# Optimization experiments

Hardware: AMD Instinct MI355X
Metric: run time of the kernel (lower is better)

The kernel has to match this reference:

```python
import jax, jax.numpy as jnp
import numpy as np

B, T, V, E, H, L = 128, 128, 5000, 256, 512, 128
PAD_IDX = 0


def setup_inputs() -> dict:
    key = jax.random.key(0)
    ks = jax.random.split(key, 12)
    s = 0.02  # init scale
    noise = jax.random.normal(ks[0], (B, L), dtype=jnp.float32)
    # Precomputed gumbel noise, one draw per (step, batch, vocab)
    u = jax.random.uniform(ks[1], (T, B, V), dtype=jnp.float32, minval=1e-9, maxval=1.0)
    gumbel = -jnp.log(-jnp.log(u))
    emb = (jax.random.normal(ks[2], (V, E), dtype=jnp.float32) * s).at[PAD_IDX].set(0.0)
    return {
        "noise": noise,
        "gumbel": gumbel,
        "temperature": jnp.float32(1.0),
        "W_init": jax.random.normal(ks[3], (H, L), dtype=jnp.float32) * s,
        "b_init": jnp.zeros((H,), dtype=jnp.float32),
        "emb": emb,
        "W_ih": jax.random.normal(ks[4], (3 * H, E), dtype=jnp.float32) * s,
        "W_hh": jax.random.normal(ks[5], (3 * H, H), dtype=jnp.float32) * s,
        "b_ih": jax.random.normal(ks[6], (3 * H,), dtype=jnp.float32) * s,
        "b_hh": jax.random.normal(ks[7], (3 * H,), dtype=jnp.float32) * s,
        "W_out": jax.random.normal(ks[8], (V, H), dtype=jnp.float32) * s,
        "b_out": jnp.zeros((V,), dtype=jnp.float32),
    }


def reference(noise, gumbel, temperature, W_init, b_init, emb, W_ih, W_hh, b_ih, b_hh, W_out, b_out):
    # h_0 = fc_initial_state(noise)  -> [B, H]
    h0 = noise @ W_init.T + b_init
    # first-step input: one-hot at pad_idx (embedding row PAD_IDX, which is zero)
    onehot0 = jnp.zeros((B, V), dtype=noise.dtype).at[:, PAD_IDX].set(1.0)
    tau = jnp.reshape(temperature, ())

    def step(carry, g):
        h, prev_onehot = carry
        x = prev_onehot @ emb                      # [B, E] soft-embedding feedback
        gi = x @ W_ih.T + b_ih                     # [B, 3H]
        gh = h @ W_hh.T + b_hh                     # [B, 3H]
        i_r, i_z, i_n = jnp.split(gi, 3, axis=-1)
        h_r, h_z, h_n = jnp.split(gh, 3, axis=-1)
        r = jax.nn.sigmoid(i_r + h_r)
        z = jax.nn.sigmoid(i_z + h_z)
        n = jnp.tanh(i_n + r * h_n)
        h_new = (1.0 - z) * n + z * h              # GRU cell (torch convention)
        # dropout is identity in eval mode
        logits = h_new @ W_out.T + b_out           # [B, V]
        y = jax.nn.softmax((logits + g) / tau, axis=-1)  # soft gumbel-softmax
        return (h_new, y), y

    _, ys = jax.lax.scan(step, (h0, onehot0), gumbel)  # ys: [T, B, V]
    return jnp.transpose(ys, (1, 0, 2))                # [B, T, V]
```

## Files before the change

kernel.cpp:

```cpp
#include <hip/hip_runtime.h>
#include <math.h>

#define Bq 128
#define Tq 128
#define Vq 5000
#define VP 5120
#define Eq 256
#define Hq 512
#define Lq 128
#define G3H 1536
#define KT 128
#define LROW 136

typedef __attribute__((ext_vector_type(8))) short bf16x8;
typedef __attribute__((ext_vector_type(4))) float f32x4;

__device__ __forceinline__ ushort f2bf(float f) {
    union { float f; unsigned u; } v; v.f = f;
    unsigned r = (v.u + 0x7FFFu + ((v.u >> 16) & 1u)) >> 16;
    return (ushort)r;
}
__device__ __forceinline__ float bf2f(ushort s) {
    union { unsigned u; float f; } v; v.u = ((unsigned)s) << 16;
    return v.f;
}

template<int MI>
__device__ __forceinline__ void macT(
    f32x4 (&acc)[MI][4],
    const ushort* __restrict__ A, int lda,
    const ushort* __restrict__ Bm, int ldb,
    int n0, int kbase, int Klen,
    ushort* As, ushort* Bs)
{
    const int NA = 2 * MI;
    const int tid = threadIdx.x;
    const int lane = tid & 63;
    const int w = tid >> 6;
    const int wm = (w >> 1) * (MI * 16);
    const int wn = (w & 1) * 64;
    const int fr = lane & 15;
    const int fk = (lane >> 4) * 8;

    int arow[NA], akc[NA];
    #pragma unroll
    for (int i = 0; i < NA; ++i) {
        int c = tid + i * 256;
        arow[i] = c >> 4; akc[i] = (c & 15) * 8;
    }
    int brow[8], bkc[8];
    #pragma unroll
    for (int i = 0; i < 8; ++i) {
        int c = tid + i * 256;
        brow[i] = c >> 4; bkc[i] = (c & 15) * 8;
    }

    const int nk = Klen / KT;
    bf16x8 ra[NA], rb[8];
    #pragma unroll
    for (int i = 0; i < NA; ++i)
        ra[i] = *(const bf16x8*)(A + (size_t)arow[i] * lda + kbase + akc[i]);
    #pragma unroll
    for (int i = 0; i < 8; ++i)
        rb[i] = *(const bf16x8*)(Bm + (size_t)(n0 + brow[i]) * ldb + kbase + bkc[i]);
    #pragma unroll
    for (int i = 0; i < NA; ++i)
        *(bf16x8*)(As + arow[i] * LROW + akc[i]) = ra[i];
    #pragma unroll
    for (int i = 0; i < 8; ++i)
        *(bf16x8*)(Bs + brow[i] * LROW + bkc[i]) = rb[i];
    __syncthreads();

    for (int kt = 0; kt < nk; ++kt) {
        if (kt + 1 < nk) {
            int kb = kbase + (kt + 1) * KT;
            #pragma unroll
            for (int i = 0; i < NA; ++i)
                ra[i] = *(const bf16x8*)(A + (size_t)arow[i] * lda + kb + akc[i]);
            #pragma unroll
            for (int i = 0; i < 8; ++i)
                rb[i] = *(const bf16x8*)(Bm + (size_t)(n0 + brow[i]) * ldb + kb + bkc[i]);
        }
        #pragma unroll
        for (int ks = 0; ks < 4; ++ks) {
            bf16x8 af[MI], bfv[4];
            const int ko = ks * 32 + fk;
            #pragma unroll
            for (int mi = 0; mi < MI; ++mi)
                af[mi] = *(const bf16x8*)(As + (wm + mi * 16 + fr) * LROW + ko);
            #pragma unroll
            for (int ni = 0; ni < 4; ++ni)
                bfv[ni] = *(const bf16x8*)(Bs + (wn + ni * 16 + fr) * LROW + ko);
            #pragma unroll
            for (int mi = 0; mi < MI; ++mi)
                #pragma unroll
                for (int ni = 0; ni < 4; ++ni)
                    acc[mi][ni] = __builtin_amdgcn_mfma_f32_16x16x32_bf16(
                        af[mi], bfv[ni], acc[mi][ni], 0, 0, 0);
        }
        __syncthreads();
        if (kt + 1 < nk) {
            #pragma unroll
            for (int i = 0; i < NA; ++i)
                *(bf16x8*)(As + arow[i] * LROW + akc[i]) = ra[i];
            #pragma unroll
            for (int i = 0; i < 8; ++i)
                *(bf16x8*)(Bs + brow[i] * LROW + bkc[i]) = rb[i];
            __syncthreads();
        }
    }
}

__global__ __launch_bounds__(256) void k_prep(
    const float* __restrict__ W_ih, const float* __restrict__ W_hh,
    const float* __restrict__ W_out, const float* __restrict__ noise,
    const float* __restrict__ W_init, const float* __restrict__ emb,
    ushort* __restrict__ WihB, ushort* __restrict__ WhhB, ushort* __restrict__ WoutB,
    ushort* __restrict__ noiseB, ushort* __restrict__ WinitB,
    ushort* __restrict__ embB, ushort* __restrict__ yE)
{
    const int tg = blockIdx.x * 256 + threadIdx.x;
    const int NTH = gridDim.x * 256;
    for (int i = tg; i < G3H * Eq / 4; i += NTH) {
        float4 f = *(const float4*)(W_ih + (size_t)i * 4);
        *(ushort4*)(WihB + (size_t)i * 4) =
            make_ushort4(f2bf(f.x), f2bf(f.y), f2bf(f.z), f2bf(f.w));
    }
    for (int i = tg; i < G3H * Hq / 4; i += NTH) {
        float4 f = *(const float4*)(W_hh + (size_t)i * 4);
        *(ushort4*)(WhhB + (size_t)i * 4) =
            make_ushort4(f2bf(f.x), f2bf(f.y), f2bf(f.z), f2bf(f.w));
    }
    for (int i = tg; i < VP * (Hq / 4); i += NTH) {
        int v = i >> 7, h4 = (i & 127) << 2;
        ushort4 o = make_ushort4(0, 0, 0, 0);
        if (v < Vq) {
            float4 f = *(const float4*)(W_out + (size_t)v * Hq + h4);
            o = make_ushort4(f2bf(f.x), f2bf(f.y), f2bf(f.z), f2bf(f.w));
        }
        *(ushort4*)(WoutB + (size_t)v * Hq + h4) = o;
    }
    for (int i = tg; i < VP * (Eq / 4); i += NTH) {
        int v = i >> 6, e4 = (i & 63) << 2;
        ushort4 o = make_ushort4(0, 0, 0, 0);
        if (v < Vq) {
            float4 f = *(const float4*)(emb + (size_t)v * Eq + e4);
            o = make_ushort4(f2bf(f.x), f2bf(f.y), f2bf(f.z), f2bf(f.w));
        }
        *(ushort4*)(embB + (size_t)v * Eq + e4) = o;
    }
    for (int i = tg; i < Bq * Lq / 4; i += NTH) {
        float4 f = *(const float4*)(noise + (size_t)i * 4);
        *(ushort4*)(noiseB + (size_t)i * 4) =
            make_ushort4(f2bf(f.x), f2bf(f.y), f2bf(f.z), f2bf(f.w));
    }
    for (int i = tg; i < Hq * Lq / 4; i += NTH) {
        float4 f = *(const float4*)(W_init + (size_t)i * 4);
        *(ushort4*)(WinitB + (size_t)i * 4) =
            make_ushort4(f2bf(f.x), f2bf(f.y), f2bf(f.z), f2bf(f.w));
    }
    for (int i = tg; i < Bq * (VP / 4); i += NTH) {
        int v4 = i % (VP / 4);
        ushort4 o = (v4 == 0) ? make_ushort4(0x3F80, 0, 0, 0)
                              : make_ushort4(0, 0, 0, 0);
        *(ushort4*)(yE + (size_t)i * 4) = o;
    }
}

__global__ __launch_bounds__(256) void k_wh0(
    const ushort* __restrict__ WihB, const ushort* __restrict__ embB,
    const ushort* __restrict__ noiseB, const ushort* __restrict__ WinitB,
    const float* __restrict__ b_init,
    ushort* __restrict__ WcombT, float* __restrict__ h0, ushort* __restrict__ hB0)
{
    __shared__ __align__(16) ushort As[128 * LROW];
    __shared__ __align__(16) ushort Bs[128 * LROW];
    const int bid = blockIdx.x;
    const int lane = threadIdx.x & 63;
    const int w = threadIdx.x >> 6;
    const int wm = (w >> 1) * 64, wn = (w & 1) * 64;
    const int fr = lane & 15, hi = lane >> 4;
    f32x4 acc[4][4];
    #pragma unroll
    for (int mi = 0; mi < 4; ++mi)
        #pragma unroll
        for (int ni = 0; ni < 4; ++ni) acc[mi][ni] = (f32x4){0.f,0.f,0.f,0.f};
    if (bid < 480) {
        int mt = bid / 40, nt = bid % 40;
        macT<4>(acc, WihB + (size_t)mt * 128 * Eq, Eq, embB, Eq,
                nt * 128, 0, Eq, As, Bs);
        #pragma unroll
        for (int mi = 0; mi < 4; ++mi)
            #pragma unroll
            for (int ni = 0; ni < 4; ++ni) {
                int n = nt * 128 + wn + ni * 16 + fr;
                #pragma unroll
                for (int r = 0; r < 4; ++r) {
                    int m = mt * 128 + wm + mi * 16 + hi * 4 + r;
                    WcombT[(size_t)m * VP + n] = f2bf(acc[mi][ni][r]);
                }
            }
    } else {
        int n0 = (bid - 480) * 128;
        macT<4>(acc, noiseB, Lq, WinitB, Lq, n0, 0, Lq, As, Bs);
        #pragma unroll
        for (int mi = 0; mi < 4; ++mi)
            #pragma unroll
            for (int ni = 0; ni < 4; ++ni) {
                int n = n0 + wn + ni * 16 + fr;
                float bv = b_init[n];
                #pragma unroll
                for (int r = 0; r < 4; ++r) {
                    int m = wm + mi * 16 + hi * 4 + r;
                    float v = acc[mi][ni][r] + bv;
                    h0[(size_t)m * Hq + n] = v;
                    hB0[(size_t)m * Hq + n] = f2bf(v);
                }
            }
    }
}

__global__ __launch_bounds__(256) void k_gi(
    const ushort* __restrict__ yE, const ushort* __restrict__ WcombT,
    const ushort* __restrict__ hB_old, const ushort* __restrict__ WhhB,
    ushort* __restrict__ gip, ushort* __restrict__ ghp,
    float* __restrict__ out, const float* __restrict__ esumAll, int t)
{
    __shared__ __align__(16) ushort As[128 * LROW];
    __shared__ __align__(16) ushort Bs[128 * LROW];
    const int bid = blockIdx.x;
    const int lane = threadIdx.x & 63, w = threadIdx.x >> 6;
    const int fr = lane & 15, hi = lane >> 4;
    if (bid < 384) {
        const int nt = bid >> 5;
        const int r5 = bid & 31;
        const int mq = r5 >> 3;
        const int z = r5 & 7;
        const int wm = (w >> 1) * 16, wn = (w & 1) * 64;
        const int n0 = nt * 128;
        f32x4 acc[1][4];
        #pragma unroll
        for (int ni = 0; ni < 4; ++ni) acc[0][ni] = (f32x4){0.f,0.f,0.f,0.f};
        macT<1>(acc, yE + (size_t)mq * 32 * VP, VP, WcombT, VP,
                n0, z * 640, 640, As, Bs);
        ushort* C = gip + (size_t)z * (Bq * G3H) + (size_t)mq * 32 * G3H;
        #pragma unroll
        for (int ni = 0; ni < 4; ++ni) {
            int n = n0 + wn + ni * 16 + fr;
            #pragma unroll
            for (int r = 0; r < 4; ++r) {
                int m = wm + hi * 4 + r;
                C[(size_t)m * G3H + n] = f2bf(acc[0][ni][r]);
            }
        }
    } else if (bid < 408) {
        const int j = bid - 384, nt = j >> 1, kc = j & 1;
        const int wm = (w >> 1) * 64, wn = (w & 1) * 64;
        const int n0 = nt * 128;
        f32x4 acc[4][4];
        #pragma unroll
        for (int mi = 0; mi < 4; ++mi)
            #pragma unroll
            for (int ni = 0; ni < 4; ++ni) acc[mi][ni] = (f32x4){0.f,0.f,0.f,0.f};
        macT<4>(acc, hB_old, Hq, WhhB, Hq, n0, kc * 256, 256, As, Bs);
        ushort* C = ghp + (size_t)kc * (Bq * G3H);
        #pragma unroll
        for (int mi = 0; mi < 4; ++mi)
            #pragma unroll
            for (int ni = 0; ni < 4; ++ni) {
                int n = n0 + wn + ni * 16 + fr;
                #pragma unroll
                for (int r = 0; r < 4; ++r) {
                    int m = wm + mi * 16 + hi * 4 + r;
                    C[(size_t)m * G3H + n] = f2bf(acc[mi][ni][r]);
                }
            }
    } else if (t > 0) {
        const int tid = threadIdx.x;
        #pragma unroll
        for (int j = 0; j < 2; ++j) {
            int b = (bid - 408) * 2 + j;
            float S = 0.f;
            #pragma unroll 8
            for (int nt = 0; nt < 40; ++nt)
                S += esumAll[(size_t)(t - 1) * 5120 + nt * 128 + b];
            float inv = 1.0f / S;
            float* orow = out + ((size_t)b * Tq + (t - 1)) * Vq;
            #pragma unroll
            for (int i = 0; i < 20; ++i) {
                int v = tid + i * 256;
                if (v < Vq) orow[v] *= inv;
            }
        }
    }
}

__global__ __launch_bounds__(256) void k_gates(
    const ushort* __restrict__ gip, const ushort* __restrict__ ghp,
    const float* __restrict__ b_ih, const float* __restrict__ b_hh,
    const float* __restrict__ h_old, const float* __restrict__ esumAll,
    float* __restrict__ h_new, ushort* __restrict__ hB_new, int t)
{
    __shared__ float sred[64];
    const int tid = threadIdx.x;
    const int e = blockIdx.x * 256 + tid;
    const int b = e >> 9, i = e & 511;
    if (t > 0) {
        if (tid < 40) sred[tid] = esumAll[(size_t)(t - 1) * 5120 + tid * 128 + b];
        __syncthreads();
        if (tid == 0) {
            float S = 0.f;
            #pragma unroll
            for (int nt = 0; nt < 40; ++nt) S += sred[nt];
            sred[63] = 1.0f / S;
        }
        __syncthreads();
    } else {
        if (tid == 0) sred[63] = 1.0f;
        __syncthreads();
    }
    const float invS = sred[63];

    const size_t o = (size_t)b * G3H + i;
    float xr = 0.f, xz = 0.f, xn = 0.f;
    #pragma unroll
    for (int z = 0; z < 8; ++z) {
        const ushort* gp = gip + (size_t)z * (Bq * G3H) + o;
        xr += bf2f(gp[0]); xz += bf2f(gp[Hq]); xn += bf2f(gp[2 * Hq]);
    }
    xr = xr * invS + b_ih[i];
    xz = xz * invS + b_ih[Hq + i];
    xn = xn * invS + b_ih[2 * Hq + i];
    const ushort* h0p = ghp + o;
    const ushort* h1p = ghp + (size_t)(Bq * G3H) + o;
    float hr = b_hh[i] + bf2f(h0p[0]) + bf2f(h1p[0]);
    float hz = b_hh[Hq + i] + bf2f(h0p[Hq]) + bf2f(h1p[Hq]);
    float hn = b_hh[2 * Hq + i] + bf2f(h0p[2 * Hq]) + bf2f(h1p[2 * Hq]);
    float r = 1.f / (1.f + expf(-(xr + hr)));
    float zz = 1.f / (1.f + expf(-(xz + hz)));
    float nn = tanhf(xn + r * hn);
    float hv = (1.f - zz) * nn + zz * h_old[e];
    h_new[e] = hv;
    hB_new[e] = f2bf(hv);
}

__global__ __launch_bounds__(256) void k_logits(
    const ushort* __restrict__ hB, const ushort* __restrict__ WoutB,
    const float* __restrict__ b_out, const float* __restrict__ gum,
    const float* __restrict__ temp,
    float* __restrict__ out, ushort* __restrict__ yE,
    float* __restrict__ esumAll, int t)
{
    __shared__ __align__(16) ushort As[32 * LROW];
    __shared__ __align__(16) ushort Bs[128 * LROW];
    const int tid = threadIdx.x;
    const int nt = blockIdx.x >> 2;
    const int mbase = (blockIdx.x & 3) * 32;
    const int n0 = nt * 128;
    const int lane = tid & 63, w = tid >> 6;
    const int wm = (w >> 1) * 16, wn = (w & 1) * 64;
    const int fr = lane & 15, hi = lane >> 4;
    const float inv_tau = 1.0f / temp[0];
    f32x4 acc[1][4];
    #pragma unroll
    for (int ni = 0; ni < 4; ++ni) acc[0][ni] = (f32x4){0.f,0.f,0.f,0.f};
    macT<1>(acc, hB + (size_t)mbase * Hq, Hq, WoutB, Hq, n0, 0, Hq, As, Bs);

    float psum[4] = {0.f, 0.f, 0.f, 0.f};
    #pragma unroll
    for (int ni = 0; ni < 4; ++ni) {
        int v = n0 + wn + ni * 16 + fr;
        bool valid = v < Vq;
        float bo = valid ? b_out[v] : 0.f;
        #pragma unroll
        for (int r = 0; r < 4; ++r) {
            int m = mbase + wm + hi * 4 + r;
            float ev = 0.f;
            if (valid) {
                float g = gum[(size_t)m * Vq + v];
                ev = expf((acc[0][ni][r] + bo + g) * inv_tau);
                out[(size_t)m * Tq * Vq + (size_t)t * Vq + v] = ev;
            }
            yE[(size_t)m * VP + v] = f2bf(ev);
            psum[r] += ev;
        }
    }
    float* redbuf = (float*)As;
    #pragma unroll
    for (int r = 0; r < 4; ++r) {
        float s = psum[r];
        s += __shfl_xor(s, 1); s += __shfl_xor(s, 2);
        s += __shfl_xor(s, 4); s += __shfl_xor(s, 8);
        if (fr == 0)
            redbuf[((wm + hi * 4 + r) << 1) | (wn >> 6)] = s;
    }
    __syncthreads();
    if (tid < 32)
        esumAll[(size_t)t * 5120 + n0 + mbase + tid]
            = redbuf[tid * 2] + redbuf[tid * 2 + 1];
}

__global__ __launch_bounds__(256) void k_tail(
    float* __restrict__ out, const float* __restrict__ esumAll)
{
    const int tid = threadIdx.x;
    #pragma unroll
    for (int j = 0; j < 4; ++j) {
        int b = blockIdx.x * 4 + j;
        float S = 0.f;
        #pragma unroll 8
        for (int nt = 0; nt < 40; ++nt)
            S += esumAll[(size_t)(Tq - 1) * 5120 + nt * 128 + b];
        float inv = 1.0f / S;
        float* orow = out + ((size_t)b * Tq + (Tq - 1)) * Vq;
        #pragma unroll
        for (int i = 0; i < 20; ++i) {
            int v = tid + i * 256;
            if (v < Vq) orow[v] *= inv;
        }
    }
}

extern "C" void kernel_launch(void* const* d_in, const int* in_sizes, int n_in,
                              void* d_out, int out_size, void* d_ws, size_t ws_size,
                              hipStream_t stream)
{
    const float* noise   = (const float*)d_in[0];
    const float* gumbel  = (const float*)d_in[1];
    const float* temp    = (const float*)d_in[2];
    const float* W_init  = (const float*)d_in[3];
    const float* b_init  = (const float*)d_in[4];
    const float* emb     = (const float*)d_in[5];
    const float* W_ih    = (const float*)d_in[6];
    const float* W_hh    = (const float*)d_in[7];
    const float* b_ih    = (const float*)d_in[8];
    const float* b_hh    = (const float*)d_in[9];
    const float* W_out   = (const float*)d_in[10];
    const float* b_out   = (const float*)d_in[11];
    float* out = (float*)d_out;

    float* fbase   = (float*)d_ws;
    float* h       = fbase;
    float* esumAll = h + 2 * 65536;
    ushort* ub     = (ushort*)(esumAll + 655360);
    ushort* gip    = ub;
    ushort* ghp    = gip + 1572864;
    ushort* embB   = ghp + 393216;
    ushort* WihB   = embB + 1310720;
    ushort* WhhB   = WihB + 393216;
    ushort* WoutB  = WhhB + 786432;
    ushort* WcombT = WoutB + 2621440;
    ushort* noiseB = WcombT + 7864320;
    ushort* WinitB = noiseB + 16384;
    ushort* hB     = WinitB + 65536;
    ushort* yE     = hB + 2 * 65536;

    k_prep<<<dim3(512), dim3(256), 0, stream>>>(
        W_ih, W_hh, W_out, noise, W_init, emb,
        WihB, WhhB, WoutB, noiseB, WinitB, embB, yE);
    k_wh0<<<dim3(484), dim3(256), 0, stream>>>(
        WihB, embB, noiseB, WinitB, b_init, WcombT, h, hB);

    for (int t = 0; t < Tq; ++t) {
        float* h_old = h + (size_t)(t & 1) * 65536;
        float* h_new = h + (size_t)((t + 1) & 1) * 65536;
        ushort* hB_old = hB + (size_t)(t & 1) * 65536;
        ushort* hB_new = hB + (size_t)((t + 1) & 1) * 65536;

        k_gi<<<dim3(472), dim3(256), 0, stream>>>(
            yE, WcombT, hB_old, WhhB, gip, ghp, out, esumAll, t);
        k_gates<<<dim3(256), dim3(256), 0, stream>>>(
            gip, ghp, b_ih, b_hh, h_old, esumAll, h_new, hB_new, t);
        k_logits<<<dim3(160), dim3(256), 0, stream>>>(
            hB_new, WoutB, b_out, gumbel + (size_t)t * Bq * Vq, temp,
            out, yE, esumAll, t);
    }
    k_tail<<<dim3(32), dim3(256), 0, stream>>>(out, esumAll);
}
```

Measured before the change: 3.513 ms.

## Move next-step hidden GEMM and prior-step normalization into logits kernel

The h@W_hh GEMM for the next step is now computed inside k_logits from the freshly produced hidden state, running alongside the output projection blocks. The deferred softmax normalization of the previous step also moves there, leaving k_gi with only the soft-embedding GEMM. Both GEMMs now use 64-row tiles instead of 32 or 128, which changes the block counts. This shortens the critical path of k_gi and fills idle CUs during k_logits, at the cost of a larger, more heterogeneous logits launch. The k_gi path for the hidden GEMM only runs at t==0.

```diff
diff --git a/kernel.cpp b/kernel.cpp
--- a/kernel.cpp
+++ b/kernel.cpp
@@ -223,75 +223,56 @@
 __global__ __launch_bounds__(256) void k_gi(
     const ushort* __restrict__ yE, const ushort* __restrict__ WcombT,
     const ushort* __restrict__ hB_old, const ushort* __restrict__ WhhB,
-    ushort* __restrict__ gip, ushort* __restrict__ ghp,
-    float* __restrict__ out, const float* __restrict__ esumAll, int t)
-{
-    __shared__ __align__(16) ushort As[128 * LROW];
+    ushort* __restrict__ gip, ushort* __restrict__ ghp, int t)
+{
+    __shared__ __align__(16) ushort As[64 * LROW];
     __shared__ __align__(16) ushort Bs[128 * LROW];
     const int bid = blockIdx.x;
     const int lane = threadIdx.x & 63, w = threadIdx.x >> 6;
     const int fr = lane & 15, hi = lane >> 4;
-    if (bid < 384) {
-        const int nt = bid >> 5;
-        const int r5 = bid & 31;
-        const int mq = r5 >> 3;
-        const int z = r5 & 7;
-        const int wm = (w >> 1) * 16, wn = (w & 1) * 64;
+    const int wm = (w >> 1) * 32, wn = (w & 1) * 64;
+    f32x4 acc[2][4];
+    #pragma unroll
+    for (int mi = 0; mi < 2; ++mi)
+        #pragma unroll
+        for (int ni = 0; ni < 4; ++ni) acc[mi][ni] = (f32x4){0.f,0.f,0.f,0.f};
+    if (bid < 192) {
+        const int nt = bid >> 4, rem = bid & 15;
+        const int mh = rem >> 3, z = rem & 7;
         const int n0 = nt * 128;
-        f32x4 acc[1][4];
-        #pragma unroll
-        for (int ni = 0; ni < 4; ++ni) acc[0][ni] = (f32x4){0.f,0.f,0.f,0.f};
-        macT<1>(acc, yE + (size_t)mq * 32 * VP, VP, WcombT, VP,
+        macT<2>(acc, yE + (size_t)mh * 64 * VP, VP, WcombT, VP,
                 n0, z * 640, 640, As, Bs);
-        ushort* C = gip + (size_t)z * (Bq * G3H) + (size_t)mq * 32 * G3H;
-        #pragma unroll
-        for (int ni = 0; ni < 4; ++ni) {
-            int n = n0 + wn + ni * 16 + fr;
-            #pragma unroll
-            for (int r = 0; r < 4; ++r) {
-                int m = wm + hi * 4 + r;
-                C[(size_t)m * G3H + n] = f2bf(acc[0][ni][r]);
-            }
-        }
-    } else if (bid < 408) {
-        const int j = bid - 384, nt = j >> 1, kc = j & 1;
-        const int wm = (w >> 1) * 64, wn = (w & 1) * 64;
-        const int n0 = nt * 128;
-        f32x4 acc[4][4];
-        #pragma unroll
-        for (int mi = 0; mi < 4; ++mi)
-            #pragma unroll
-            for (int ni = 0; ni < 4; ++ni) acc[mi][ni] = (f32x4){0.f,0.f,0.f,0.f};
-        macT<4>(acc, hB_old, Hq, WhhB, Hq, n0, kc * 256, 256, As, Bs);
-        ushort* C = ghp + (size_t)kc * (Bq * G3H);
-        #pragma unroll
-        for (int mi = 0; mi < 4; ++mi)
+        ushort* C = gip + (size_t)z * (Bq * G3H);
+        #pragma unroll
+        for (int mi = 0; mi < 2; ++mi)
             #pragma unroll
             for (int ni = 0; ni < 4; ++ni) {
                 int n = n0 + wn + ni * 16 + fr;
                 #pragma unroll
                 for (int r = 0; r < 4; ++r) {
-                    int m = wm + mi * 16 + hi * 4 + r;
+                    int m = mh * 64 + wm + mi * 16 + hi * 4 + r;
                     C[(size_t)m * G3H + n] = f2bf(acc[mi][ni][r]);
                 }
             }
-    } else if (t > 0) {
-        const int tid = threadIdx.x;
-        #pragma unroll
-        for (int j = 0; j < 2; ++j) {
-            int b = (bid - 408) * 2 + j;
-            float S = 0.f;
-            #pragma unroll 8
-            for (int nt = 0; nt < 40; ++nt)
-                S += esumAll[(size_t)(t - 1) * 5120 + nt * 128 + b];
-            float inv = 1.0f / S;
-            float* orow = out + ((size_t)b * Tq + (t - 1)) * Vq;
-            #pragma unroll
-            for (int i = 0; i < 20; ++i) {
-                int v = tid + i * 256;
-                if (v < Vq) orow[v] *= inv;
-            }
-        }
+    } else if (t == 0) {
+        const int j = bid - 192;
+        const int nt = j >> 2, rem = j & 3;
+        const int mh = rem >> 1, kc = rem & 1;
+        const int n0 = nt * 128;
+        macT<2>(acc, hB_old + (size_t)mh * 64 * Hq, Hq, WhhB, Hq,
+                n0, kc * 256, 256, As, Bs);
+        ushort* C = ghp + (size_t)kc * (Bq * G3H);
+        #pragma unroll
+        for (int mi = 0; mi < 2; ++mi)
+            #pragma unroll
+            for (int ni = 0; ni < 4; ++ni) {
+                int n = n0 + wn + ni * 16 + fr;
+                #pragma unroll
+                for (int r = 0; r < 4; ++r) {
+                    int m = mh * 64 + wm + mi * 16 + hi * 4 + r;
+                    C[(size_t)m * G3H + n] = f2bf(acc[mi][ni][r]);
+                }
+            }
     }
 }
 
@@ -346,58 +327,103 @@
 
 __global__ __launch_bounds__(256) void k_logits(
     const ushort* __restrict__ hB, const ushort* __restrict__ WoutB,
+    const ushort* __restrict__ WhhB,
     const float* __restrict__ b_out, const float* __restrict__ gum,
     const float* __restrict__ temp,
     float* __restrict__ out, ushort* __restrict__ yE,
-    float* __restrict__ esumAll, int t)
-{
-    __shared__ __align__(16) ushort As[32 * LROW];
+    float* __restrict__ esumAll, ushort* __restrict__ ghp, int t)
+{
+    __shared__ __align__(16) ushort As[64 * LROW];
     __shared__ __align__(16) ushort Bs[128 * LROW];
+    const int bid = blockIdx.x;
     const int tid = threadIdx.x;
-    const int nt = blockIdx.x >> 2;
-    const int mbase = (blockIdx.x & 3) * 32;
-    const int n0 = nt * 128;
     const int lane = tid & 63, w = tid >> 6;
-    const int wm = (w >> 1) * 16, wn = (w & 1) * 64;
     const int fr = lane & 15, hi = lane >> 4;
-    const float inv_tau = 1.0f / temp[0];
-    f32x4 acc[1][4];
-    #pragma unroll
-    for (int ni = 0; ni < 4; ++ni) acc[0][ni] = (f32x4){0.f,0.f,0.f,0.f};
-    macT<1>(acc, hB + (size_t)mbase * Hq, Hq, WoutB, Hq, n0, 0, Hq, As, Bs);
-
-    float psum[4] = {0.f, 0.f, 0.f, 0.f};
-    #pragma unroll
-    for (int ni = 0; ni < 4; ++ni) {
-        int v = n0 + wn + ni * 16 + fr;
-        bool valid = v < Vq;
-        float bo = valid ? b_out[v] : 0.f;
+    if (bid < 160) {
+        const int nt = bid >> 2;
+        const int mbase = (bid & 3) * 32;
+        const int n0 = nt * 128;
+        const int wm = (w >> 1) * 16, wn = (w & 1) * 64;
+        const float inv_tau = 1.0f / temp[0];
+        f32x4 acc[1][4];
+        #pragma unroll
+        for (int ni = 0; ni < 4; ++ni) acc[0][ni] = (f32x4){0.f,0.f,0.f,0.f};
+        macT<1>(acc, hB + (size_t)mbase * Hq, Hq, WoutB, Hq, n0, 0, Hq, As, Bs);
+
+        float psum[4] = {0.f, 0.f, 0.f, 0.f};
+        #pragma unroll
+        for (int ni = 0; ni < 4; ++ni) {
+            int v = n0 + wn + ni * 16 + fr;
+            bool valid = v < Vq;
+            float bo = valid ? b_out[v] : 0.f;
+            #pragma unroll
+            for (int r = 0; r < 4; ++r) {
+                int m = mbase + wm + hi * 4 + r;
+                float ev = 0.f;
+                if (valid) {
+                    float g = gum[(size_t)m * Vq + v];
+                    ev = expf((acc[0][ni][r] + bo + g) * inv_tau);
+                    out[(size_t)m * Tq * Vq + (size_t)t * Vq + v] = ev;
+                }
+                yE[(size_t)m * VP + v] = f2bf(ev);
+                psum[r] += ev;
+            }
+        }
+        float* redbuf = (float*)As;
         #pragma unroll
         for (int r = 0; r < 4; ++r) {
-            int m = mbase + wm + hi * 4 + r;
-            float ev = 0.f;
-            if (valid) {
-                float g = gum[(size_t)m * Vq + v];
-                ev = expf((acc[0][ni][r] + bo + g) * inv_tau);
-                out[(size_t)m * Tq * Vq + (size_t)t * Vq + v] = ev;
-            }
-            yE[(size_t)m * VP + v] = f2bf(ev);
-            psum[r] += ev;
-        }
-    }
-    float* redbuf = (float*)As;
-    #pragma unroll
-    for (int r = 0; r < 4; ++r) {
-        float s = psum[r];
-        s += __shfl_xor(s, 1); s += __shfl_xor(s, 2);
-        s += __shfl_xor(s, 4); s += __shfl_xor(s, 8);
-        if (fr == 0)
-            redbuf[((wm + hi * 4 + r) << 1) | (wn >> 6)] = s;
-    }
-    __syncthreads();
-    if (tid < 32)
-        esumAll[(size_t)t * 5120 + n0 + mbase + tid]
-            = redbuf[tid * 2] + redbuf[tid * 2 + 1];
+            float s = psum[r];
+            s += __shfl_xor(s, 1); s += __shfl_xor(s, 2);
+            s += __shfl_xor(s, 4); s += __shfl_xor(s, 8);
+            if (fr == 0)
+                redbuf[((wm + hi * 4 + r) << 1) | (wn >> 6)] = s;
+        }
+        __syncthreads();
+        if (tid < 32)
+            esumAll[(size_t)t * 5120 + n0 + mbase + tid]
+                = redbuf[tid * 2] + redbuf[tid * 2 + 1];
+    } else if (bid < 208) {
+        const int j = bid - 160;
+        const int nt = j >> 2, rem = j & 3;
+        const int mh = rem >> 1, kc = rem & 1;
+        const int n0 = nt * 128;
+        const int wm = (w >> 1) * 32, wn = (w & 1) * 64;
+        f32x4 acc[2][4];
+        #pragma unroll
+        for (int mi = 0; mi < 2; ++mi)
+            #pragma unroll
+            for (int ni = 0; ni < 4; ++ni) acc[mi][ni] = (f32x4){0.f,0.f,0.f,0.f};
+        macT<2>(acc, hB + (size_t)mh * 64 * Hq, Hq, WhhB, Hq,
+                n0, kc * 256, 256, As, Bs);
+        ushort* C = ghp + (size_t)kc * (Bq * G3H);
+        #pragma unroll
+        for (int mi = 0; mi < 2; ++mi)
+            #pragma unroll
+            for (int ni = 0; ni < 4; ++ni) {
+                int n = n0 + wn + ni * 16 + fr;
+                #pragma unroll
+                for (int r = 0; r < 4; ++r) {
+                    int m = mh * 64 + wm + mi * 16 + hi * 4 + r;
+                    C[(size_t)m * G3H + n] = f2bf(acc[mi][ni][r]);
+                }
+            }
+    } else if (t > 0) {
+        #pragma unroll
+        for (int j = 0; j < 2; ++j) {
+            int b = (bid - 208) * 2 + j;
+            float S = 0.f;
+            #pragma unroll 8
+            for (int nt2 = 0; nt2 < 40; ++nt2)
+                S += esumAll[(size_t)(t - 1) * 5120 + nt2 * 128 + b];
+            float inv = 1.0f / S;
+            float* orow = out + ((size_t)b * Tq + (t - 1)) * Vq;
+            #pragma unroll
+            for (int i = 0; i < 20; ++i) {
+                int v = tid + i * 256;
+                if (v < Vq) orow[v] *= inv;
+            }
+        }
+    }
 }
 
 __global__ __launch_bounds__(256) void k_tail(
@@ -467,13 +493,13 @@
         ushort* hB_old = hB + (size_t)(t & 1) * 65536;
         ushort* hB_new = hB + (size_t)((t + 1) & 1) * 65536;
 
-        k_gi<<<dim3(472), dim3(256), 0, stream>>>(
-            yE, WcombT, hB_old, WhhB, gip, ghp, out, esumAll, t);
+        k_gi<<<dim3(t == 0 ? 240 : 192), dim3(256), 0, stream>>>(
+            yE, WcombT, hB_old, WhhB, gip, ghp, t);
         k_gates<<<dim3(256), dim3(256), 0, stream>>>(
             gip, ghp, b_ih, b_hh, h_old, esumAll, h_new, hB_new, t);
-        k_logits<<<dim3(160), dim3(256), 0, stream>>>(
-            hB_new, WoutB, b_out, gumbel + (size_t)t * Bq * Vq, temp,
-            out, yE, esumAll, t);
+        k_logits<<<dim3(272), dim3(256), 0, stream>>>(
+            hB_new, WoutB, WhhB, b_out, gumbel + (size_t)t * Bq * Vq, temp,
+            out, yE, esumAll, ghp, t);
     }
     k_tail<<<dim3(32), dim3(256), 0, stream>>>(out, esumAll);
 }
```

Result: no change. 3.583 ms (+2.0%).

## Fuse GRU gates into logits kernel via in-kernel atomic barrier

Applied to the files above, without the earlier changes.

Merges the gate-update kernel into the logits kernel: 8 blocks compute the GRU state and signal through an atomic counter, while the 160 logits blocks spin-wait on per-group flags before running their GEMM. This removes one kernel launch per timestep (128 in total). The W_hh GEMM is also split across more, smaller blocks (48 instead of 24), with a smaller shared-memory A tile. The risk is that the spin-wait deadlocks or stalls if the producer blocks are not co-resident. The gate work is also concentrated in only 8 blocks, so that phase gets less parallelism.

```diff
diff --git a/kernel.cpp b/kernel.cpp
--- a/kernel.cpp
+++ b/kernel.cpp
@@ -111,6 +111,234 @@
     }
 }
 
+
+__device__ __forceinline__ void gi_block(
+    int bid, const ushort* __restrict__ yE, const ushort* __restrict__ WcombT,
+    ushort* __restrict__ gip, ushort* As, ushort* Bs)
+{
+    const int tid = threadIdx.x;
+    const int lane = tid & 63, w = tid >> 6;
+    const int fr = lane & 15, hi = lane >> 4;
+    const int nt = bid >> 5, rem = bid & 31;
+    const int mq = rem >> 3, z = rem & 7;
+    const int wm = (w >> 1) * 16, wn = (w & 1) * 64;
+    const int n0 = nt * 128;
+    f32x4 acc[1][4];
+    #pragma unroll
+    for (int ni = 0; ni < 4; ++ni) acc[0][ni] = (f32x4){0.f,0.f,0.f,0.f};
+    macT<1>(acc, yE + (size_t)mq * 32 * VP, VP, WcombT, VP,
+            n0, z * 640, 640, As, Bs);
+    ushort* C = gip + (size_t)z * (Bq * G3H) + (size_t)mq * 32 * G3H;
+    #pragma unroll
+    for (int ni = 0; ni < 4; ++ni) {
+        int n = n0 + wn + ni * 16 + fr;
+        #pragma unroll
+        for (int r = 0; r < 4; ++r) {
+            int m = wm + hi * 4 + r;
+            C[(size_t)m * G3H + n] = f2bf(acc[0][ni][r]);
+        }
+    }
+}
+
+__device__ __forceinline__ void gh_block(
+    int j, const ushort* __restrict__ hBsrc, const ushort* __restrict__ WhhB,
+    ushort* __restrict__ ghp, ushort* As, ushort* Bs)
+{
+    const int tid = threadIdx.x;
+    const int lane = tid & 63, w = tid >> 6;
+    const int fr = lane & 15, hi = lane >> 4;
+    const int nt = j >> 2, rem = j & 3;
+    const int mh = rem >> 1, kc = rem & 1;
+    const int n0 = nt * 128;
+    const int wm = (w >> 1) * 32, wn = (w & 1) * 64;
+    f32x4 acc[2][4];
+    #pragma unroll
+    for (int mi = 0; mi < 2; ++mi)
+        #pragma unroll
+        for (int ni = 0; ni < 4; ++ni) acc[mi][ni] = (f32x4){0.f,0.f,0.f,0.f};
+    macT<2>(acc, hBsrc + (size_t)mh * 64 * Hq, Hq, WhhB, Hq,
+            n0, kc * 256, 256, As, Bs);
+    ushort* C = ghp + (size_t)kc * (Bq * G3H);
+    #pragma unroll
+    for (int mi = 0; mi < 2; ++mi)
+        #pragma unroll
+        for (int ni = 0; ni < 4; ++ni) {
+            int n = n0 + wn + ni * 16 + fr;
+            #pragma unroll
+            for (int r = 0; r < 4; ++r) {
+                int m = mh * 64 + wm + mi * 16 + hi * 4 + r;
+                C[(size_t)m * G3H + n] = f2bf(acc[mi][ni][r]);
+            }
+        }
+}
+
+__device__ __forceinline__ void norm2(
+    int bpair, int tprev, float* __restrict__ out,
+    const float* __restrict__ esumAll)
+{
+    const int tid = threadIdx.x;
+    #pragma unroll
+    for (int j = 0; j < 2; ++j) {
+        int b = bpair * 2 + j;
+        float S = 0.f;
+        #pragma unroll 8
+        for (int nt = 0; nt < 40; ++nt)
+            S += esumAll[(size_t)tprev * 5120 + nt * 128 + b];
+        float inv = 1.0f / S;
+        float* orow = out + ((size_t)b * Tq + tprev) * Vq;
+        #pragma unroll
+        for (int i = 0; i < 20; ++i) {
+            int v = tid + i * 256;
+            if (v < Vq) orow[v] *= inv;
+        }
+    }
+}
+
+__global__ __launch_bounds__(256) void k_s1(
+    const ushort* __restrict__ yE, const ushort* __restrict__ WcombT,
+    const ushort* __restrict__ hB_old, const ushort* __restrict__ WhhB,
+    ushort* __restrict__ gip, ushort* __restrict__ ghp,
+    float* __restrict__ out, const float* __restrict__ esumAll, int t)
+{
+    __shared__ __align__(16) ushort As[64 * LROW];
+    __shared__ __align__(16) ushort Bs[128 * LROW];
+    const int bid = blockIdx.x;
+    if (bid < 384)
+        gi_block(bid, yE, WcombT, gip, As, Bs);
+    else if (bid < 432)
+        gh_block(bid - 384, hB_old, WhhB, ghp, As, Bs);
+    else if (t > 0)
+        norm2(bid - 432, t - 1, out, esumAll);
+}
+
+__global__ __launch_bounds__(256) void k_gl(
+    const ushort* __restrict__ gip, const ushort* __restrict__ ghp,
+    const float* __restrict__ b_ih, const float* __restrict__ b_hh,
+    const float* __restrict__ h_old, float* __restrict__ h_new,
+    ushort* __restrict__ hB_new,
+    const ushort* __restrict__ WoutB, const float* __restrict__ b_out,
+    const float* __restrict__ gum, const float* __restrict__ temp,
+    float* __restrict__ out, ushort* __restrict__ yE,
+    float* __restrict__ esumAll, unsigned* __restrict__ bar, int t)
+{
+    __shared__ __align__(16) ushort As[32 * LROW];
+    __shared__ __align__(16) ushort Bs[128 * LROW];
+    __shared__ float invS_sh[16];
+    const int tid = threadIdx.x;
+    const int bid = blockIdx.x;
+
+    if (bid < 8) {
+        const int b0 = bid * 16;
+        if (t > 0) {
+            if (tid < 16) {
+                float S = 0.f;
+                #pragma unroll 8
+                for (int q = 0; q < 40; ++q)
+                    S += esumAll[(size_t)(t - 1) * 5120 + q * 128 + (b0 + tid)];
+                invS_sh[tid] = 1.0f / S;
+            }
+        } else if (tid < 16) {
+            invS_sh[tid] = 1.0f;
+        }
+        __syncthreads();
+        for (int k = 0; k < 32; ++k) {
+            const int el = k * 256 + tid;
+            const int lb = el >> 9, i = el & 511;
+            const int b = b0 + lb;
+            const int e = b * 512 + i;
+            const float invS = invS_sh[lb];
+            const size_t o = (size_t)b * G3H + i;
+            float xr = 0.f, xz = 0.f, xn = 0.f;
+            #pragma unroll
+            for (int z = 0; z < 8; ++z) {
+                const ushort* gp = gip + (size_t)z * (Bq * G3H) + o;
+                xr += bf2f(gp[0]); xz += bf2f(gp[Hq]); xn += bf2f(gp[2 * Hq]);
+            }
+            xr = xr * invS + b_ih[i];
+            xz = xz * invS + b_ih[Hq + i];
+            xn = xn * invS + b_ih[2 * Hq + i];
+            const ushort* h0p = ghp + o;
+            const ushort* h1p = ghp + (size_t)(Bq * G3H) + o;
+            float hr = b_hh[i] + bf2f(h0p[0]) + bf2f(h1p[0]);
+            float hz = b_hh[Hq + i] + bf2f(h0p[Hq]) + bf2f(h1p[Hq]);
+            float hn = b_hh[2 * Hq + i] + bf2f(h0p[2 * Hq]) + bf2f(h1p[2 * Hq]);
+            float r = 1.f / (1.f + expf(-(xr + hr)));
+            float zz = 1.f / (1.f + expf(-(xz + hz)));
+            float nn = tanhf(xn + r * hn);
+            float hv = (1.f - zz) * nn + zz * h_old[e];
+            h_new[e] = hv;
+            hB_new[e] = f2bf(hv);
+        }
+        __syncthreads();
+        if (tid == 0) {
+            unsigned r = __hip_atomic_fetch_add(bar, 1u, __ATOMIC_ACQ_REL,
+                                                __HIP_MEMORY_SCOPE_AGENT);
+            if (r == (unsigned)(8 * t + 7)) {
+                #pragma unroll
+                for (int q = 0; q < 8; ++q)
+                    __hip_atomic_store(bar + 32 * (q + 1), (unsigned)(t + 1),
+                                       __ATOMIC_RELEASE, __HIP_MEMORY_SCOPE_AGENT);
+            }
+        }
+        return;
+    }
+
+    const int gidx = bid - 8;
+    const int nt = gidx % 40;
+    const int mbase = (gidx / 40) * 32;
+    if (tid == 0) {
+        unsigned* rep = bar + 32 * ((gidx & 7) + 1);
+        while (__hip_atomic_load(rep, __ATOMIC_RELAXED,
+                                 __HIP_MEMORY_SCOPE_AGENT) < (unsigned)(t + 1))
+            __builtin_amdgcn_s_sleep(2);
+        (void)__hip_atomic_load(rep, __ATOMIC_ACQUIRE, __HIP_MEMORY_SCOPE_AGENT);
+    }
+    __syncthreads();
+
+    const int lane = tid & 63, w = tid >> 6;
+    const int fr = lane & 15, hi = lane >> 4;
+    const int n0 = nt * 128;
+    const int wm = (w >> 1) * 16, wn = (w & 1) * 64;
+    const float inv_tau = 1.0f / temp[0];
+    f32x4 acc[1][4];
+    #pragma unroll
+    for (int ni = 0; ni < 4; ++ni) acc[0][ni] = (f32x4){0.f,0.f,0.f,0.f};
+    macT<1>(acc, hB_new + (size_t)mbase * Hq, Hq, WoutB, Hq, n0, 0, Hq, As, Bs);
+
+    float psum[4] = {0.f, 0.f, 0.f, 0.f};
+    #pragma unroll
+    for (int ni = 0; ni < 4; ++ni) {
+        int v = n0 + wn + ni * 16 + fr;
+        bool valid = v < Vq;
+        float bo = valid ? b_out[v] : 0.f;
+        #pragma unroll
+        for (int r = 0; r < 4; ++r) {
+            int m = mbase + wm + hi * 4 + r;
+            float ev = 0.f;
+            if (valid) {
+                float g = gum[(size_t)m * Vq + v];
+                ev = expf((acc[0][ni][r] + bo + g) * inv_tau);
+                out[(size_t)m * Tq * Vq + (size_t)t * Vq + v] = ev;
+            }
+            yE[(size_t)m * VP + v] = f2bf(ev);
+            psum[r] += ev;
+        }
+    }
+    float* redbuf = (float*)As;
+    #pragma unroll
+    for (int r = 0; r < 4; ++r) {
+        float s = psum[r];
+        s += __shfl_xor(s, 1); s += __shfl_xor(s, 2);
+        s += __shfl_xor(s, 4); s += __shfl_xor(s, 8);
+        if (fr == 0)
+            redbuf[((wm + hi * 4 + r) << 1) | (wn >> 6)] = s;
+    }
+    __syncthreads();
+    if (tid < 32)
+        esumAll[(size_t)t * 5120 + n0 + mbase + tid]
+            = redbuf[tid * 2] + redbuf[tid * 2 + 1];
+}
+
 __global__ __launch_bounds__(256) void k_prep(
     const float* __restrict__ W_ih, const float* __restrict__ W_hh,
     const float* __restrict__ W_out, const float* __restrict__ noise,
@@ -220,205 +448,15 @@
     }
 }
 
-__global__ __launch_bounds__(256) void k_gi(
-    const ushort* __restrict__ yE, const ushort* __restrict__ WcombT,
-    const ushort* __restrict__ hB_old, const ushort* __restrict__ WhhB,
-    ushort* __restrict__ gip, ushort* __restrict__ ghp,
-    float* __restrict__ out, const float* __restrict__ esumAll, int t)
-{
-    __shared__ __align__(16) ushort As[128 * LROW];
-    __shared__ __align__(16) ushort Bs[128 * LROW];
-    const int bid = blockIdx.x;
-    const int lane = threadIdx.x & 63, w = threadIdx.x >> 6;
-    const int fr = lane & 15, hi = lane >> 4;
-    if (bid < 384) {
-        const int nt = bid >> 5;
-        const int r5 = bid & 31;
-        const int mq = r5 >> 3;
-        const int z = r5 & 7;
-        const int wm = (w >> 1) * 16, wn = (w & 1) * 64;
-        const int n0 = nt * 128;
-        f32x4 acc[1][4];
-        #pragma unroll
-        for (int ni = 0; ni < 4; ++ni) acc[0][ni] = (f32x4){0.f,0.f,0.f,0.f};
-        macT<1>(acc, yE + (size_t)mq * 32 * VP, VP, WcombT, VP,
-                n0, z * 640, 640, As, Bs);
-        ushort* C = gip + (size_t)z * (Bq * G3H) + (size_t)mq * 32 * G3H;
-        #pragma unroll
-        for (int ni = 0; ni < 4; ++ni) {
-            int n = n0 + wn + ni * 16 + fr;
-            #pragma unroll
-            for (int r = 0; r < 4; ++r) {
-                int m = wm + hi * 4 + r;
-                C[(size_t)m * G3H + n] = f2bf(acc[0][ni][r]);
-            }
-        }
-    } else if (bid < 408) {
-        const int j = bid - 384, nt = j >> 1, kc = j & 1;
-        const int wm = (w >> 1) * 64, wn = (w & 1) * 64;
-        const int n0 = nt * 128;
-        f32x4 acc[4][4];
-        #pragma unroll
-        for (int mi = 0; mi < 4; ++mi)
-            #pragma unroll
-            for (int ni = 0; ni < 4; ++ni) acc[mi][ni] = (f32x4){0.f,0.f,0.f,0.f};
-        macT<4>(acc, hB_old, Hq, WhhB, Hq, n0, kc * 256, 256, As, Bs);
-        ushort* C = ghp + (size_t)kc * (Bq * G3H);
-        #pragma unroll
-        for (int mi = 0; mi < 4; ++mi)
-            #pragma unroll
-            for (int ni = 0; ni < 4; ++ni) {
-                int n = n0 + wn + ni * 16 + fr;
-                #pragma unroll
-                for (int r = 0; r < 4; ++r) {
-                    int m = wm + mi * 16 + hi * 4 + r;
-                    C[(size_t)m * G3H + n] = f2bf(acc[mi][ni][r]);
-                }
-            }
-    } else if (t > 0) {
-        const int tid = threadIdx.x;
-        #pragma unroll
-        for (int j = 0; j < 2; ++j) {
-            int b = (bid - 408) * 2 + j;
-            float S = 0.f;
-            #pragma unroll 8
-            for (int nt = 0; nt < 40; ++nt)
-                S += esumAll[(size_t)(t - 1) * 5120 + nt * 128 + b];
-            float inv = 1.0f / S;
-            float* orow = out + ((size_t)b * Tq + (t - 1)) * Vq;
-            #pragma unroll
-            for (int i = 0; i < 20; ++i) {
-                int v = tid + i * 256;
-                if (v < Vq) orow[v] *= inv;
-            }
-        }
-    }
-}
-
-__global__ __launch_bounds__(256) void k_gates(
-    const ushort* __restrict__ gip, const ushort* __restrict__ ghp,
-    const float* __restrict__ b_ih, const float* __restrict__ b_hh,
-    const float* __restrict__ h_old, const float* __restrict__ esumAll,
-    float* __restrict__ h_new, ushort* __restrict__ hB_new, int t)
-{
-    __shared__ float sred[64];
-    const int tid = threadIdx.x;
-    const int e = blockIdx.x * 256 + tid;
-    const int b = e >> 9, i = e & 511;
-    if (t > 0) {
-        if (tid < 40) sred[tid] = esumAll[(size_t)(t - 1) * 5120 + tid * 128 + b];
-        __syncthreads();
-        if (tid == 0) {
-            float S = 0.f;
-            #pragma unroll
-            for (int nt = 0; nt < 40; ++nt) S += sred[nt];
-            sred[63] = 1.0f / S;
-        }
-        __syncthreads();
-    } else {
-        if (tid == 0) sred[63] = 1.0f;
-        __syncthreads();
-    }
-    const float invS = sred[63];
-
-    const size_t o = (size_t)b * G3H + i;
-    float xr = 0.f, xz = 0.f, xn = 0.f;
-    #pragma unroll
-    for (int z = 0; z < 8; ++z) {
-        const ushort* gp = gip + (size_t)z * (Bq * G3H) + o;
-        xr += bf2f(gp[0]); xz += bf2f(gp[Hq]); xn += bf2f(gp[2 * Hq]);
-    }
-    xr = xr * invS + b_ih[i];
-    xz = xz * invS + b_ih[Hq + i];
-    xn = xn * invS + b_ih[2 * Hq + i];
-    const ushort* h0p = ghp + o;
-    const ushort* h1p = ghp + (size_t)(Bq * G3H) + o;
-    float hr = b_hh[i] + bf2f(h0p[0]) + bf2f(h1p[0]);
-    float hz = b_hh[Hq + i] + bf2f(h0p[Hq]) + bf2f(h1p[Hq]);
-    float hn = b_hh[2 * Hq + i] + bf2f(h0p[2 * Hq]) + bf2f(h1p[2 * Hq]);
-    float r = 1.f / (1.f + expf(-(xr + hr)));
-    float zz = 1.f / (1.f + expf(-(xz + hz)));
-    float nn = tanhf(xn + r * hn);
-    float hv = (1.f - zz) * nn + zz * h_old[e];
-    h_new[e] = hv;
-    hB_new[e] = f2bf(hv);
-}
-
-__global__ __launch_bounds__(256) void k_logits(
-    const ushort* __restrict__ hB, const ushort* __restrict__ WoutB,
-    const float* __restrict__ b_out, const float* __restrict__ gum,
-    const float* __restrict__ temp,
-    float* __restrict__ out, ushort* __restrict__ yE,
-    float* __restrict__ esumAll, int t)
-{
-    __shared__ __align__(16) ushort As[32 * LROW];
-    __shared__ __align__(16) ushort Bs[128 * LROW];
-    const int tid = threadIdx.x;
-    const int nt = blockIdx.x >> 2;
-    const int mbase = (blockIdx.x & 3) * 32;
-    const int n0 = nt * 128;
-    const int lane = tid & 63, w = tid >> 6;
-    const int wm = (w >> 1) * 16, wn = (w & 1) * 64;
-    const int fr = lane & 15, hi = lane >> 4;
-    const float inv_tau = 1.0f / temp[0];
-    f32x4 acc[1][4];
-    #pragma unroll
-    for (int ni = 0; ni < 4; ++ni) acc[0][ni] = (f32x4){0.f,0.f,0.f,0.f};
-    macT<1>(acc, hB + (size_t)mbase * Hq, Hq, WoutB, Hq, n0, 0, Hq, As, Bs);
-
-    float psum[4] = {0.f, 0.f, 0.f, 0.f};
-    #pragma unroll
-    for (int ni = 0; ni < 4; ++ni) {
-        int v = n0 + wn + ni * 16 + fr;
-        bool valid = v < Vq;
-        float bo = valid ? b_out[v] : 0.f;
-        #pragma unroll
-        for (int r = 0; r < 4; ++r) {
-            int m = mbase + wm + hi * 4 + r;
-            float ev = 0.f;
-            if (valid) {
-                float g = gum[(size_t)m * Vq + v];
-                ev = expf((acc[0][ni][r] + bo + g) * inv_tau);
-                out[(size_t)m * Tq * Vq + (size_t)t * Vq + v] = ev;
-            }
-            yE[(size_t)m * VP + v] = f2bf(ev);
-            psum[r] += ev;
-        }
-    }
-    float* redbuf = (float*)As;
-    #pragma unroll
-    for (int r = 0; r < 4; ++r) {
-        float s = psum[r];
-        s += __shfl_xor(s, 1); s += __shfl_xor(s, 2);
-        s += __shfl_xor(s, 4); s += __shfl_xor(s, 8);
-        if (fr == 0)
-            redbuf[((wm + hi * 4 + r) << 1) | (wn >> 6)] = s;
-    }
-    __syncthreads();
-    if (tid < 32)
-        esumAll[(size_t)t * 5120 + n0 + mbase + tid]
-            = redbuf[tid * 2] + redbuf[tid * 2 + 1];
+__global__ void k_zero(unsigned* __restrict__ bar)
+{
+    if (threadIdx.x < 512) bar[threadIdx.x] = 0u;
 }
 
 __global__ __launch_bounds__(256) void k_tail(
     float* __restrict__ out, const float* __restrict__ esumAll)
 {
-    const int tid = threadIdx.x;
-    #pragma unroll
-    for (int j = 0; j < 4; ++j) {
-        int b = blockIdx.x * 4 + j;
-        float S = 0.f;
-        #pragma unroll 8
-        for (int nt = 0; nt < 40; ++nt)
-            S += esumAll[(size_t)(Tq - 1) * 5120 + nt * 128 + b];
-        float inv = 1.0f / S;
-        float* orow = out + ((size_t)b * Tq + (Tq - 1)) * Vq;
-        #pragma unroll
-        for (int i = 0; i < 20; ++i) {
-            int v = tid + i * 256;
-            if (v < Vq) orow[v] *= inv;
-        }
-    }
+    norm2(blockIdx.x, Tq - 1, out, esumAll);
 }
 
 extern "C" void kernel_launch(void* const* d_in, const int* in_sizes, int n_in,
@@ -455,11 +493,14 @@
     ushort* hB     = WinitB + 65536;
     ushort* yE     = hB + 2 * 65536;
 
+    unsigned* bar = (unsigned*)noiseB;
+
     k_prep<<<dim3(512), dim3(256), 0, stream>>>(
         W_ih, W_hh, W_out, noise, W_init, emb,
         WihB, WhhB, WoutB, noiseB, WinitB, embB, yE);
     k_wh0<<<dim3(484), dim3(256), 0, stream>>>(
         WihB, embB, noiseB, WinitB, b_init, WcombT, h, hB);
+    k_zero<<<dim3(1), dim3(512), 0, stream>>>(bar);
 
     for (int t = 0; t < Tq; ++t) {
         float* h_old = h + (size_t)(t & 1) * 65536;
@@ -467,13 +508,12 @@
         ushort* hB_old = hB + (size_t)(t & 1) * 65536;
         ushort* hB_new = hB + (size_t)((t + 1) & 1) * 65536;
 
-        k_gi<<<dim3(472), dim3(256), 0, stream>>>(
+        k_s1<<<dim3(t == 0 ? 432 : 496), dim3(256), 0, stream>>>(
             yE, WcombT, hB_old, WhhB, gip, ghp, out, esumAll, t);
-        k_gates<<<dim3(256), dim3(256), 0, stream>>>(
-            gip, ghp, b_ih, b_hh, h_old, esumAll, h_new, hB_new, t);
-        k_logits<<<dim3(160), dim3(256), 0, stream>>>(
-            hB_new, WoutB, b_out, gumbel + (size_t)t * Bq * Vq, temp,
-            out, yE, esumAll, t);
-    }
-    k_tail<<<dim3(32), dim3(256), 0, stream>>>(out, esumAll);
-}
+        k_gl<<<dim3(168), dim3(256), 0, stream>>>(
+            gip, ghp, b_ih, b_hh, h_old, h_new, hB_new,
+            WoutB, b_out, gumbel + (size_t)t * Bq * Vq, temp,
+            out, yE, esumAll, bar, t);
+    }
+    k_tail<<<dim3(64), dim3(256), 0, stream>>>(out, esumAll);
+}
```

New measurement: 7.252 ms. +106.4%, slower.
